# Optimization experiments

Measured on AMD Instinct MI355X. Metric: run time of the kernel, lower is better.

Reference implementation:

```python
import jax, jax.numpy as jnp
import numpy as np

FISTA_ITER = 50
LAMBDA = 0.1
POWER_ITER = 100


def power_method(W):
    # Estimates c = largest eigenvalue of W^T W (squared spectral norm).
    # Torch code uses a random init vector; we use a fixed key for determinism.
    X0 = jax.random.normal(jax.random.key(1), (1, W.shape[1]), dtype=W.dtype)

    def body(i, carry):
        X, _ = carry
        X = (X @ W.T) @ W            # [1, m]
        nm = jnp.linalg.norm(X)
        return (X / nm, nm)

    _, nm = jax.lax.fori_loop(0, POWER_ITER, body, (X0, jnp.asarray(1.0, W.dtype)))
    return nm


def soft_threshold(X, lam):
    return jnp.sign(X) * jax.nn.relu(jnp.abs(X) - lam)


def fista(Y, W, lam, iters):
    c = power_method(W)
    eta = 1.0 / c
    Gamma0 = soft_threshold(Y @ (eta * W), lam)   # [B, m]
    Y_norm = jnp.linalg.norm(Y)
    t0 = jnp.asarray(1.0, Y.dtype)

    def step(carry, _):
        Gamma, Z, t = carry
        residual = Z @ W.T - Y                                   # [B, n]
        Gamma_new = soft_threshold(Z - eta * (residual @ W), lam / c)
        t_new = (1.0 + jnp.sqrt(1.0 + 4.0 * t ** 2)) / 2.0
        Z_new = Gamma_new + (t - 1.0) / t_new * (Gamma_new - Gamma)
        nrm = jnp.linalg.norm(residual) / Y_norm
        return (Gamma_new, Z_new, t_new), nrm

    (Gamma, _, _), norms = jax.lax.scan(step, (Gamma0, Gamma0, t0), None, length=iters)
    return Gamma, norms


def setup_inputs() -> dict:
    key = jax.random.key(0)
    k1, k2 = jax.random.split(key)
    Y = jax.random.normal(k1, (8192, 784), dtype=jnp.float32)
    W = jax.random.normal(k2, (784, 2048), dtype=jnp.float32)
    W = W / jnp.linalg.norm(W, axis=0, keepdims=True)  # NormDict
    return {"Y": Y, "W": W}


def reference(Y, W):
    Gamma, norms = fista(Y, W, LAMBDA, FISTA_ITER)
    X = Gamma @ W.T                  # reconstruction [B, 784]
    return (X, Gamma, norms)
```

## Files before the change

kernel.cpp:

```cpp
#include <hip/hip_runtime.h>
#include <math.h>

#define B_DIM   8192
#define N_DIM   784
#define NPAD    800
#define NROWS_W 1024
#define M_DIM   2048
#define XSZ     (B_DIM*N_DIM)
#define GSZ     (B_DIM*M_DIM)
#define NITER   50
#define PITER   100

typedef __attribute__((ext_vector_type(8))) short short8;
typedef __attribute__((ext_vector_type(4))) float floatx4;

__device__ __forceinline__ void async_ld16(const unsigned short* g, unsigned short* l){
  __builtin_amdgcn_global_load_lds(
      (const __attribute__((address_space(1))) unsigned int*)g,
      (__attribute__((address_space(3))) unsigned int*)l,
      16, 0, 0);
}

__device__ __forceinline__ unsigned rotl32(unsigned x, int d){ return (x<<d)|(x>>(32-d)); }

__device__ void threefry2x32(unsigned& v0, unsigned& v1){
  const unsigned ks0=0u, ks1=1u, ks2=0x1BD11BDBu;
  unsigned x0=v0+ks0, x1=v1+ks1;
#define RND(R) { x0+=x1; x1=rotl32(x1,R); x1^=x0; }
  RND(13) RND(15) RND(26) RND(6)
  x0+=ks1; x1+=ks2+1u;
  RND(17) RND(29) RND(16) RND(24)
  x0+=ks2; x1+=ks0+2u;
  RND(13) RND(15) RND(26) RND(6)
  x0+=ks0; x1+=ks1+3u;
  RND(17) RND(29) RND(16) RND(24)
  x0+=ks1; x1+=ks2+4u;
  RND(13) RND(15) RND(26) RND(6)
  x0+=ks2; x1+=ks0+5u;
#undef RND
  v0=x0; v1=x1;
}

__device__ float erfinv_f(float x){
  float w = -logf((1.0f-x)*(1.0f+x));
  float p;
  if (w < 5.0f){
    w -= 2.5f;
    p = 2.81022636e-08f;
    p = fmaf(p,w, 3.43273939e-07f);
    p = fmaf(p,w,-3.5233877e-06f);
    p = fmaf(p,w,-4.39150654e-06f);
    p = fmaf(p,w, 0.00021858087f);
    p = fmaf(p,w,-0.00125372503f);
    p = fmaf(p,w,-0.00417768164f);
    p = fmaf(p,w, 0.246640727f);
    p = fmaf(p,w, 1.50140941f);
  } else {
    w = sqrtf(w) - 3.0f;
    p = -0.000200214257f;
    p = fmaf(p,w, 0.000100950558f);
    p = fmaf(p,w, 0.00134934322f);
    p = fmaf(p,w,-0.00367342844f);
    p = fmaf(p,w, 0.00573950773f);
    p = fmaf(p,w,-0.0076224613f);
    p = fmaf(p,w, 0.00943887047f);
    p = fmaf(p,w, 1.00167406f);
    p = fmaf(p,w, 2.83297682f);
  }
  return p*x;
}

__device__ float bits_to_normal(unsigned b){
  unsigned fb = (b>>9) | 0x3f800000u;
  float u01 = __uint_as_float(fb) - 1.0f;
  const float lo = -0.99999994f;
  float u = u01*(1.0f - lo) + lo;
  u = fmaxf(lo, u);
  return 1.41421356237f * erfinv_f(u);
}

__global__ void setup_kernel(float* __restrict__ xbuf0, float* __restrict__ accs){
  int i = threadIdx.x;
  if (i < 64) accs[i] = 0.0f;
  unsigned v0 = (unsigned)i, v1 = (unsigned)(1024+i);
  threefry2x32(v0, v1);
  xbuf0[i]        = bits_to_normal(v0);
  xbuf0[1024 + i] = bits_to_normal(v1);
}

__device__ __forceinline__ unsigned short f2bf(float f){
  unsigned u = __float_as_uint(f);
  unsigned r = (u + 0x7fffu + ((u>>16)&1u)) >> 16;
  return (unsigned short)r;
}
__device__ __forceinline__ unsigned pack2(float a, float b){
  return (unsigned)f2bf(a) | ((unsigned)f2bf(b) << 16);
}
__device__ __forceinline__ float bf2f(unsigned short s){
  return __uint_as_float(((unsigned)s) << 16);
}

__global__ void conv_w(const float* __restrict__ W, unsigned short* __restrict__ Wbf){
  int i4 = (blockIdx.x*256 + threadIdx.x)*4;
  int row = i4 >> 11;
  uint2 p = make_uint2(0,0);
  if (row < N_DIM){
    float4 v = *(const float4*)(W + (size_t)row*M_DIM + (i4 & 2047));
    p.x = pack2(v.x, v.y); p.y = pack2(v.z, v.w);
  }
  *(uint2*)(Wbf + i4) = p;
}

__global__ void conv_y(const float* __restrict__ Y, unsigned short* __restrict__ Ybf){
  int row = blockIdx.x;
  int c4 = threadIdx.x*4;
  if (c4 >= NPAD) return;
  uint2 p = make_uint2(0,0);
  if (c4 < N_DIM){
    float4 v = *(const float4*)(Y + (size_t)row*N_DIM + c4);
    p.x = pack2(v.x, v.y); p.y = pack2(v.z, v.w);
  }
  *(uint2*)(Ybf + (size_t)row*NPAD + c4) = p;
}

__global__ void transpose_w(const float* __restrict__ W, unsigned short* __restrict__ WTbf){
  __shared__ float tile[32][33];
  int k0 = blockIdx.x*32;
  int j0 = blockIdx.y*32;
  int tx = threadIdx.x & 31, ty = threadIdx.x >> 5;
#pragma unroll
  for (int i=0;i<4;i++){
    int j = j0 + ty + 8*i;
    float v = (j < N_DIM) ? W[(size_t)j*M_DIM + k0 + tx] : 0.0f;
    tile[tx][ty+8*i] = v;
  }
  __syncthreads();
#pragma unroll
  for (int i=0;i<4;i++){
    int k = k0 + ty + 8*i;
    WTbf[(size_t)k*NPAD + j0 + tx] = f2bf(tile[ty+8*i][tx]);
  }
}

__global__ __launch_bounds__(256)
void compute_q(const float* __restrict__ W, float* __restrict__ Q){
  __shared__ float As2[16][132];
  __shared__ float Bs2[16][132];
  const int t = threadIdx.x;
  const int a0 = blockIdx.x*128, b0 = blockIdx.y*128;
  const int ty = t>>4, tx = t&15;
  float acc[8][8];
#pragma unroll
  for (int i=0;i<8;i++)
#pragma unroll
    for (int j=0;j<8;j++) acc[i][j]=0.0f;

  for (int j0=0; j0<N_DIM; j0+=16){
#pragma unroll
    for (int h=0; h<8; ++h){
      int idx = h*256 + t;
      int r = idx>>7, c = idx&127;
      As2[r][c] = W[(size_t)(j0+r)*M_DIM + a0 + c];
      Bs2[r][c] = W[(size_t)(j0+r)*M_DIM + b0 + c];
    }
    __syncthreads();
#pragma unroll
    for (int kk=0; kk<16; ++kk){
      float a[8], b[8];
#pragma unroll
      for (int i=0;i<8;i++) a[i] = As2[kk][ty*8+i];
#pragma unroll
      for (int j=0;j<8;j++) b[j] = Bs2[kk][tx*8+j];
#pragma unroll
      for (int i=0;i<8;i++)
#pragma unroll
        for (int j=0;j<8;j++) acc[i][j] = fmaf(a[i], b[j], acc[i][j]);
    }
    __syncthreads();
  }
#pragma unroll
  for (int i=0;i<8;i++){
    int a = a0 + ty*8 + i;
#pragma unroll
    for (int j=0;j<8;j++) Q[(size_t)a*M_DIM + b0 + tx*8 + j] = acc[i][j];
  }
}

__global__ void sumsq_kernel(const float* __restrict__ v, int n, float* __restrict__ acc){
  __shared__ float red[256];
  int t = threadIdx.x;
  float s = 0.0f;
  for (int i = blockIdx.x*256 + t; i < n; i += gridDim.x*256){ float x = v[i]; s = fmaf(x,x,s); }
  red[t] = s; __syncthreads();
  for (int off=128; off>0; off>>=1){ if (t<off) red[t]+=red[t+off]; __syncthreads(); }
  if (t==0) atomicAdd(acc, red[0]);
}

__global__ void pm_q(const float* __restrict__ x, const float* __restrict__ Q,
                     float* __restrict__ xout){
  __shared__ float red[256];
  int t = threadIdx.x;
  float s = 0.0f;
  for (int k=t; k<M_DIM; k+=256){ float v = x[k]; s = fmaf(v,v,s); }
  red[t]=s; __syncthreads();
  for (int off=128; off>0; off>>=1){ if (t<off) red[t]+=red[t+off]; __syncthreads(); }
  float inv = 1.0f/sqrtf(red[0]);
  int wave = t>>6, lane = t&63;
  int j = blockIdx.x*4 + wave;
  const float* Qr = Q + (size_t)j*M_DIM;
  float acc = 0.0f;
  for (int k=lane; k<M_DIM; k+=64) acc = fmaf(x[k], Qr[k], acc);
  for (int off=32; off>0; off>>=1) acc += __shfl_down(acc, off);
  if (lane==0) xout[j] = acc * inv;
}

__global__ void finish_power(const float* __restrict__ xfin, const float* __restrict__ accs,
                             float* __restrict__ params){
  __shared__ float red[256];
  int t = threadIdx.x;
  float s = 0.0f;
  for (int k=t; k<M_DIM; k+=256){ float v = xfin[k]; s = fmaf(v,v,s); }
  red[t]=s; __syncthreads();
  for (int off=128; off>0; off>>=1){ if (t<off) red[t]+=red[t+off]; __syncthreads(); }
  if (t==0){
    float c = sqrtf(red[0]);
    params[0] = c;
    params[1] = 1.0f/c;
    params[2] = 0.1f/c;
    params[3] = sqrtf(accs[0]);
  }
}

__device__ __forceinline__ float softthr(float v, float th){
  float a = fmaxf(fabsf(v) - th, 0.0f);
  return copysignf(a, v);
}

template<int MODE>
__global__ __launch_bounds__(256)
void mfma_nt(const unsigned short* __restrict__ Abf,
             const unsigned short* __restrict__ Bbf,
             const float* __restrict__ Y,
             unsigned short* __restrict__ Rbf,
             float* __restrict__ X,
             float* __restrict__ nacc){
  __shared__ float4 smem4[2560];
  unsigned short* As0 = (unsigned short*)smem4;
  unsigned short* Bs0 = As0 + 64*32;
  unsigned short* As1 = Bs0 + 256*32;
  unsigned short* Bs1 = As1 + 64*32;
  float* fbuf = (float*)smem4;

  const int bid = blockIdx.x;
  const int g8  = bid & 7, w = bid >> 3;
  const int m0  = (g8*16 + (w>>2))*64;
  const int n0  = (w & 3)*256;

  const int t    = threadIdx.x;
  const int wave = t>>6, lane = t&63;
  const int wm2  = wave>>1, wn2 = wave&1;
  const int quad = lane>>4, l15 = lane&15;
  const int lrow = lane>>2;
  const int lk   = (lane&3)*8;

  floatx4 acc[2][8];
#pragma unroll
  for (int i=0;i<2;i++)
#pragma unroll
    for (int j=0;j<8;j++) acc[i][j] = (floatx4)(0.0f);

  auto stage = [&](unsigned short* As, unsigned short* Bs, int k0){
    async_ld16(Abf + (size_t)(m0 + wave*16 + lrow)*M_DIM + k0 + lk, &As[wave*512]);
#pragma unroll
    for (int c=0; c<4; ++c){
      int chunk = wave*4 + c;
      async_ld16(Bbf + (size_t)(n0 + chunk*16 + lrow)*M_DIM + k0 + lk, &Bs[chunk*512]);
    }
  };

  stage(As0, Bs0, 0);
  __syncthreads();
  int cur = 0;
  for (int k0=0; k0<M_DIM; k0+=32, cur^=1){
    unsigned short* As = cur ? As1 : As0;
    unsigned short* Bs = cur ? Bs1 : Bs0;
    if (k0+32 < M_DIM) stage(cur ? As0 : As1, cur ? Bs0 : Bs1, k0+32);
    short8 af[2], bfr[8];
#pragma unroll
    for (int ti=0; ti<2; ++ti)
      af[ti] = *(const short8*)&As[(wm2*32 + ti*16 + l15)*32 + quad*8];
#pragma unroll
    for (int tj=0; tj<8; ++tj)
      bfr[tj] = *(const short8*)&Bs[(wn2*128 + tj*16 + l15)*32 + quad*8];
#pragma unroll
    for (int ti=0; ti<2; ++ti)
#pragma unroll
      for (int tj=0; tj<8; ++tj)
        acc[ti][tj] = __builtin_amdgcn_mfma_f32_16x16x32_bf16(af[ti], bfr[tj], acc[ti][tj], 0, 0, 0);
    __syncthreads();
  }

  float ss = 0.0f;
#pragma unroll
  for (int c=0; c<4; ++c){
    if (wn2 == (c>>1)){
      int tb = (c&1)*4;
#pragma unroll
      for (int ti=0; ti<2; ++ti)
#pragma unroll
        for (int u=0; u<4; ++u)
#pragma unroll
          for (int r=0; r<4; ++r)
            fbuf[(wm2*32 + ti*16 + quad*4 + r)*68 + u*16 + l15] = acc[ti][tb+u][r];
    }
    __syncthreads();
#pragma unroll
    for (int k=0; k<4; ++k){
      int row = k*16 + (t>>4);
      int col = (t&15)*4;
      int m = m0 + row;
      int n = n0 + c*64 + col;
      float4 v = *(const float4*)&fbuf[row*68 + col];
      if (MODE==0){
        if (n < N_DIM){
          float4 yv = *(const float4*)(Y + (size_t)m*N_DIM + n);
          float r0 = v.x - yv.x, r1 = v.y - yv.y, r2 = v.z - yv.z, r3 = v.w - yv.w;
          uint2 p; p.x = pack2(r0, r1); p.y = pack2(r2, r3);
          *(uint2*)(Rbf + (size_t)m*NPAD + n) = p;
          ss = fmaf(r0,r0, fmaf(r1,r1, fmaf(r2,r2, fmaf(r3,r3, ss))));
        } else if (n < NPAD){
          *(uint2*)(Rbf + (size_t)m*NPAD + n) = make_uint2(0,0);
        }
      } else {
        if (n < N_DIM) *(float4*)(X + (size_t)m*N_DIM + n) = v;
      }
    }
    __syncthreads();
  }

  if (MODE==0){
    for (int off=32; off>0; off>>=1) ss += __shfl_down(ss, off);
    if (lane==0) atomicAdd(nacc, ss);
  }
}

template<int MODE>
__global__ __launch_bounds__(256,3)
void mfma_nn(const unsigned short* __restrict__ Abf,
             const unsigned short* __restrict__ WTbf,
             float* __restrict__ Gamma,
             unsigned short* __restrict__ Zhi,
             unsigned short* __restrict__ Zlo,
             const float* __restrict__ params,
             float mu){
  __shared__ float4 smem4[2048];
  unsigned short* As0 = (unsigned short*)smem4;
  unsigned short* Bs0 = As0 + 128*32;
  unsigned short* As1 = Bs0 + 128*32;
  unsigned short* Bs1 = As1 + 128*32;
  float* fbuf = (float*)smem4;

  const int bid = blockIdx.x;
  const int g8  = bid & 7, w = bid >> 3;
  const int m0  = (g8*8 + (w>>4))*128;
  const int n0  = (w & 15)*128;

  const int t    = threadIdx.x;
  const int wave = t>>6, lane = t&63;
  const int wm   = wave>>1, wn = wave&1;
  const int quad = lane>>4, l15 = lane&15;
  const int lrow = lane>>2;
  const int lk   = (lane&3)*8;

  floatx4 acc[4][4];
#pragma unroll
  for (int i=0;i<4;i++)
#pragma unroll
    for (int j=0;j<4;j++) acc[i][j] = (floatx4)(0.0f);

  auto stage = [&](unsigned short* As, unsigned short* Bs, int k0){
#pragma unroll
    for (int c=0; c<2; ++c){
      int chunk = wave*2 + c;
      async_ld16(Abf  + (size_t)(m0 + chunk*16 + lrow)*NPAD + k0 + lk, &As[chunk*512]);
      async_ld16(WTbf + (size_t)(n0 + chunk*16 + lrow)*NPAD + k0 + lk, &Bs[chunk*512]);
    }
  };

  stage(As0, Bs0, 0);
  __syncthreads();
  int cur = 0;
  for (int k0=0; k0<NPAD; k0+=32, cur^=1){
    unsigned short* As = cur ? As1 : As0;
    unsigned short* Bs = cur ? Bs1 : Bs0;
    if (k0+32 < NPAD) stage(cur ? As0 : As1, cur ? Bs0 : Bs1, k0+32);
    short8 af[4], bfr[4];
#pragma unroll
    for (int ti=0; ti<4; ++ti)
      af[ti] = *(const short8*)&As[(wm*64 + ti*16 + l15)*32 + quad*8];
#pragma unroll
    for (int tj=0; tj<4; ++tj)
      bfr[tj] = *(const short8*)&Bs[(wn*64 + tj*16 + l15)*32 + quad*8];
#pragma unroll
    for (int ti=0; ti<4; ++ti)
#pragma unroll
      for (int tj=0; tj<4; ++tj)
        acc[ti][tj] = __builtin_amdgcn_mfma_f32_16x16x32_bf16(af[ti], bfr[tj], acc[ti][tj], 0, 0, 0);
    __syncthreads();
  }

  const float eta  = params[1];
  const float lamc = params[2];

#pragma unroll
  for (int c=0; c<4; ++c){
    if (wn == (c>>1)){
      int tb = (c&1)*2;
#pragma unroll
      for (int ti=0; ti<4; ++ti)
#pragma unroll
        for (int u=0; u<2; ++u)
#pragma unroll
          for (int r=0; r<4; ++r)
            fbuf[(wm*64 + ti*16 + quad*4 + r)*36 + u*16 + l15] = acc[ti][tb+u][r];
    }
    __syncthreads();
    const int rbase = t>>3;
    const int col   = (t&7)*4;
    const int n     = n0 + c*32 + col;
    size_t idx[4];
    uint2 ph[4], pl[4];
    float4 gov[4];
#pragma unroll
    for (int k=0; k<4; ++k){
      int m = m0 + k*32 + rbase;
      idx[k] = (size_t)m*M_DIM + n;
      if (MODE!=0){
        ph[k] = *(const uint2*)(Zhi + idx[k]);
        pl[k] = *(const uint2*)(Zlo + idx[k]);
      }
      if (MODE==1) gov[k] = *(const float4*)(Gamma + idx[k]);
    }
#pragma unroll
    for (int k=0; k<4; ++k){
      int row = k*32 + rbase;
      float4 g4 = *(const float4*)&fbuf[row*36 + col];
      float gr[4] = {g4.x, g4.y, g4.z, g4.w};
      if (MODE!=0){
        unsigned short h[4] = {(unsigned short)(ph[k].x&0xffff),(unsigned short)(ph[k].x>>16),
                               (unsigned short)(ph[k].y&0xffff),(unsigned short)(ph[k].y>>16)};
        unsigned short l[4] = {(unsigned short)(pl[k].x&0xffff),(unsigned short)(pl[k].x>>16),
                               (unsigned short)(pl[k].y&0xffff),(unsigned short)(pl[k].y>>16)};
#pragma unroll
        for (int e=0;e<4;e++){
          float zv = bf2f(h[e]) + bf2f(l[e]);
          gr[e] = softthr(zv - eta*gr[e], lamc);
        }
      } else {
#pragma unroll
        for (int e=0;e<4;e++) gr[e] = softthr(eta*gr[e], 0.1f);
      }
      *(float4*)(Gamma + idx[k]) = make_float4(gr[0],gr[1],gr[2],gr[3]);
      if (MODE==1){
        float go0 = gov[k].x, go1 = gov[k].y, go2 = gov[k].z, go3 = gov[k].w;
        float zn[4];
        zn[0] = gr[0] + mu*(gr[0] - go0);
        zn[1] = gr[1] + mu*(gr[1] - go1);
        zn[2] = gr[2] + mu*(gr[2] - go2);
        zn[3] = gr[3] + mu*(gr[3] - go3);
        unsigned short h0=f2bf(zn[0]), h1=f2bf(zn[1]), h2=f2bf(zn[2]), h3=f2bf(zn[3]);
        uint2 phx; phx.x = (unsigned)h0 | ((unsigned)h1<<16); phx.y = (unsigned)h2 | ((unsigned)h3<<16);
        uint2 plx; plx.x = pack2(zn[0]-bf2f(h0), zn[1]-bf2f(h1));
                   plx.y = pack2(zn[2]-bf2f(h2), zn[3]-bf2f(h3));
        *(uint2*)(Zhi + idx[k]) = phx;
        *(uint2*)(Zlo + idx[k]) = plx;
      } else if (MODE==0){
        unsigned short h0=f2bf(gr[0]), h1=f2bf(gr[1]), h2=f2bf(gr[2]), h3=f2bf(gr[3]);
        uint2 phx; phx.x = (unsigned)h0 | ((unsigned)h1<<16); phx.y = (unsigned)h2 | ((unsigned)h3<<16);
        uint2 plx; plx.x = pack2(gr[0]-bf2f(h0), gr[1]-bf2f(h1));
                   plx.y = pack2(gr[2]-bf2f(h2), gr[3]-bf2f(h3));
        *(uint2*)(Zhi + idx[k]) = phx;
        *(uint2*)(Zlo + idx[k]) = plx;
      } else {
        uint2 phx; phx.x = pack2(gr[0], gr[1]); phx.y = pack2(gr[2], gr[3]);
        *(uint2*)(Zhi + idx[k]) = phx;
      }
    }
    __syncthreads();
  }
}

__global__ void norms_finalize(const float* __restrict__ nacc, const float* __restrict__ params,
                               float* __restrict__ out){
  int i = threadIdx.x;
  if (i < NITER) out[i] = sqrtf(nacc[i]) / params[3];
}

extern "C" void kernel_launch(void* const* d_in, const int* in_sizes, int n_in,
                              void* d_out, int out_size, void* d_ws, size_t ws_size,
                              hipStream_t stream){
  const float* Y  = (const float*)d_in[0];
  const float* W  = (const float*)d_in[1];
  float* out      = (float*)d_out;
  float* X        = out;
  float* Gamma    = out + XSZ;
  float* norms    = out + XSZ + GSZ;

  unsigned short* Zhi  = (unsigned short*)d_ws;
  unsigned short* Zlo  = Zhi  + (size_t)GSZ;
  unsigned short* Rbf  = Zlo  + (size_t)GSZ;
  unsigned short* Wbf  = Rbf  + (size_t)B_DIM*NPAD;
  unsigned short* WTbf = Wbf  + (size_t)NROWS_W*M_DIM;
  float* Q      = (float*)(WTbf + (size_t)M_DIM*NPAD);
  float* xb0    = Q + (size_t)M_DIM*M_DIM;
  float* xb1    = xb0 + M_DIM;
  float* params = xb1 + M_DIM;
  float* accs   = params + 8;

  setup_kernel<<<dim3(1), dim3(1024), 0, stream>>>(xb0, accs);
  sumsq_kernel<<<dim3(512), dim3(256), 0, stream>>>(Y, XSZ, accs);
  conv_w      <<<dim3(2048), dim3(256), 0, stream>>>(W, Wbf);
  transpose_w <<<dim3(64,25), dim3(256), 0, stream>>>(W, WTbf);
  conv_y      <<<dim3(B_DIM), dim3(256), 0, stream>>>(Y, Rbf);

  compute_q<<<dim3(16,16), dim3(256), 0, stream>>>(W, Q);
  float* xa = xb0; float* xc = xb1;
  for (int it=0; it<PITER; ++it){
    pm_q<<<dim3(512), dim3(256), 0, stream>>>(xa, Q, xc);
    float* tmp = xa; xa = xc; xc = tmp;
  }
  finish_power<<<dim3(1), dim3(256), 0, stream>>>(xa, accs, params);

  mfma_nn<0><<<dim3(1024), dim3(256), 0, stream>>>(Rbf, WTbf, Gamma, Zhi, Zlo, params, 0.0f);

  float tcur = 1.0f;
  for (int it=0; it<NITER; ++it){
    mfma_nt<0><<<dim3(512), dim3(256), 0, stream>>>(Zhi, Wbf, Y, Rbf, nullptr, accs + 1 + it);
    float tsq = tcur*tcur;
    float tn  = (1.0f + sqrtf(1.0f + 4.0f*tsq)) / 2.0f;
    float mu  = (tcur - 1.0f) / tn;
    tcur = tn;
    if (it < NITER-1)
      mfma_nn<1><<<dim3(1024), dim3(256), 0, stream>>>(Rbf, WTbf, Gamma, Zhi, Zlo, params, mu);
    else
      mfma_nn<2><<<dim3(1024), dim3(256), 0, stream>>>(Rbf, WTbf, Gamma, Zhi, Zlo, params, mu);
  }

  norms_finalize<<<dim3(1), dim3(64), 0, stream>>>(accs + 1, params, norms);

  mfma_nt<1><<<dim3(512), dim3(256), 0, stream>>>(Zhi, Wbf, nullptr, nullptr, X, nullptr);
}
```

Baseline: 8.316 ms.

## Shrink power-method Gram matrix, swizzle LDS tiles, keep fp32 Z/Gamma in fragment layout

The power method now iterates on the 784x784 matrix W W^T instead of the 2048x2048 W^T W. It tracks the Rayleigh quotient through atomics, so each iteration no longer needs its own norm reduction. Both MFMA GEMMs use an XOR swizzle on the LDS k-offset to cut bank conflicts. The FISTA epilogue keeps fp32 Z and Gamma in a per-thread fragment layout (Gamma scratch lives in the output buffer), which removes the LDS transpose and the hi/lo bf16 split except in the final iteration. The costs are scattered 2-byte Zhi stores and a different eigenvalue estimator whose numerics may differ slightly.

```diff
diff --git a/kernel.cpp b/kernel.cpp
--- a/kernel.cpp
+++ b/kernel.cpp
@@ -79,9 +79,11 @@
   return 1.41421356237f * erfinv_f(u);
 }
 
-__global__ void setup_kernel(float* __restrict__ xbuf0, float* __restrict__ accs){
+__global__ void setup_kernel(float* __restrict__ xbuf0, float* __restrict__ accs,
+                             float* __restrict__ dbuf){
   int i = threadIdx.x;
   if (i < 64) accs[i] = 0.0f;
+  if (i < 128) dbuf[i] = (i==0) ? 1.0f : 0.0f;
   unsigned v0 = (unsigned)i, v1 = (unsigned)(1024+i);
   threefry2x32(v0, v1);
   xbuf0[i]        = bits_to_normal(v0);
@@ -143,47 +145,91 @@
 }
 
 __global__ __launch_bounds__(256)
-void compute_q(const float* __restrict__ W, float* __restrict__ Q){
-  __shared__ float As2[16][132];
-  __shared__ float Bs2[16][132];
+void compute_qp(const float* __restrict__ W, float* __restrict__ Qp){
+  __shared__ float As2[64][33];
+  __shared__ float Bs2[64][33];
   const int t = threadIdx.x;
-  const int a0 = blockIdx.x*128, b0 = blockIdx.y*128;
+  const int a0 = blockIdx.x*64, b0 = blockIdx.y*64;
   const int ty = t>>4, tx = t&15;
-  float acc[8][8];
-#pragma unroll
-  for (int i=0;i<8;i++)
-#pragma unroll
-    for (int j=0;j<8;j++) acc[i][j]=0.0f;
-
-  for (int j0=0; j0<N_DIM; j0+=16){
-#pragma unroll
-    for (int h=0; h<8; ++h){
-      int idx = h*256 + t;
-      int r = idx>>7, c = idx&127;
-      As2[r][c] = W[(size_t)(j0+r)*M_DIM + a0 + c];
-      Bs2[r][c] = W[(size_t)(j0+r)*M_DIM + b0 + c];
-    }
-    __syncthreads();
-#pragma unroll
-    for (int kk=0; kk<16; ++kk){
-      float a[8], b[8];
-#pragma unroll
-      for (int i=0;i<8;i++) a[i] = As2[kk][ty*8+i];
-#pragma unroll
-      for (int j=0;j<8;j++) b[j] = Bs2[kk][tx*8+j];
-#pragma unroll
-      for (int i=0;i<8;i++)
-#pragma unroll
-        for (int j=0;j<8;j++) acc[i][j] = fmaf(a[i], b[j], acc[i][j]);
-    }
-    __syncthreads();
-  }
-#pragma unroll
-  for (int i=0;i<8;i++){
-    int a = a0 + ty*8 + i;
-#pragma unroll
-    for (int j=0;j<8;j++) Q[(size_t)a*M_DIM + b0 + tx*8 + j] = acc[i][j];
-  }
+  float acc[4][4];
+#pragma unroll
+  for (int i=0;i<4;i++)
+#pragma unroll
+    for (int j=0;j<4;j++) acc[i][j]=0.0f;
+
+  for (int k0=0; k0<M_DIM; k0+=32){
+#pragma unroll
+    for (int h=0; h<2; ++h){
+      int row = h*32 + (t>>3);
+      int kq  = (t&7)*4;
+      float4 av = make_float4(0,0,0,0), bv = make_float4(0,0,0,0);
+      if (a0+row < N_DIM) av = *(const float4*)(W + (size_t)(a0+row)*M_DIM + k0 + kq);
+      if (b0+row < N_DIM) bv = *(const float4*)(W + (size_t)(b0+row)*M_DIM + k0 + kq);
+      As2[row][kq]=av.x; As2[row][kq+1]=av.y; As2[row][kq+2]=av.z; As2[row][kq+3]=av.w;
+      Bs2[row][kq]=bv.x; Bs2[row][kq+1]=bv.y; Bs2[row][kq+2]=bv.z; Bs2[row][kq+3]=bv.w;
+    }
+    __syncthreads();
+#pragma unroll
+    for (int kk=0; kk<32; ++kk){
+      float a[4], b[4];
+#pragma unroll
+      for (int i=0;i<4;i++) a[i] = As2[ty*4+i][kk];
+#pragma unroll
+      for (int j=0;j<4;j++) b[j] = Bs2[tx*4+j][kk];
+#pragma unroll
+      for (int i=0;i<4;i++)
+#pragma unroll
+        for (int j=0;j<4;j++) acc[i][j] = fmaf(a[i], b[j], acc[i][j]);
+    }
+    __syncthreads();
+  }
+#pragma unroll
+  for (int i=0;i<4;i++){
+    int a = a0 + ty*4 + i;
+    if (a >= N_DIM) continue;
+#pragma unroll
+    for (int j=0;j<4;j++){
+      int b = b0 + tx*4 + j;
+      if (b < N_DIM) Qp[(size_t)a*N_DIM + b] = acc[i][j];
+    }
+  }
+}
+
+__global__ void u0_kernel(const float* __restrict__ x0, const float* __restrict__ W,
+                          float* __restrict__ u0){
+  int wave = threadIdx.x>>6, lane = threadIdx.x&63;
+  int j = blockIdx.x*4 + wave;
+  const float* Wr = W + (size_t)j*M_DIM;
+  float s = 0.0f;
+  for (int k=lane; k<M_DIM; k+=64) s = fmaf(x0[k], Wr[k], s);
+  for (int off=32; off>0; off>>=1) s += __shfl_down(s, off);
+  if (lane==0) u0[j] = s;
+}
+
+__global__ void pm_qp(const float* __restrict__ vin, const float* __restrict__ din,
+                      const float* __restrict__ Qp,
+                      float* __restrict__ vout, float* __restrict__ dout){
+  int wave = threadIdx.x>>6, lane = threadIdx.x&63;
+  int j = blockIdx.x*4 + wave;
+  float inv = 1.0f/sqrtf(*din);
+  const float* Qr = Qp + (size_t)j*N_DIM;
+  float s = 0.0f;
+  for (int k=lane; k<N_DIM; k+=64) s = fmaf(vin[k], Qr[k], s);
+  for (int off=32; off>0; off>>=1) s += __shfl_down(s, off);
+  if (lane==0){
+    float w = s * inv;
+    vout[j] = w;
+    atomicAdd(dout, w * vin[j] * inv);
+  }
+}
+
+__global__ void finish_power2(const float* __restrict__ d100, const float* __restrict__ accs,
+                              float* __restrict__ params){
+  float c = sqrtf(*d100);
+  params[0] = c;
+  params[1] = 1.0f/c;
+  params[2] = 0.1f/c;
+  params[3] = sqrtf(accs[0]);
 }
 
 __global__ void sumsq_kernel(const float* __restrict__ v, int n, float* __restrict__ acc){
@@ -194,41 +240,6 @@
   red[t] = s; __syncthreads();
   for (int off=128; off>0; off>>=1){ if (t<off) red[t]+=red[t+off]; __syncthreads(); }
   if (t==0) atomicAdd(acc, red[0]);
-}
-
-__global__ void pm_q(const float* __restrict__ x, const float* __restrict__ Q,
-                     float* __restrict__ xout){
-  __shared__ float red[256];
-  int t = threadIdx.x;
-  float s = 0.0f;
-  for (int k=t; k<M_DIM; k+=256){ float v = x[k]; s = fmaf(v,v,s); }
-  red[t]=s; __syncthreads();
-  for (int off=128; off>0; off>>=1){ if (t<off) red[t]+=red[t+off]; __syncthreads(); }
-  float inv = 1.0f/sqrtf(red[0]);
-  int wave = t>>6, lane = t&63;
-  int j = blockIdx.x*4 + wave;
-  const float* Qr = Q + (size_t)j*M_DIM;
-  float acc = 0.0f;
-  for (int k=lane; k<M_DIM; k+=64) acc = fmaf(x[k], Qr[k], acc);
-  for (int off=32; off>0; off>>=1) acc += __shfl_down(acc, off);
-  if (lane==0) xout[j] = acc * inv;
-}
-
-__global__ void finish_power(const float* __restrict__ xfin, const float* __restrict__ accs,
-                             float* __restrict__ params){
-  __shared__ float red[256];
-  int t = threadIdx.x;
-  float s = 0.0f;
-  for (int k=t; k<M_DIM; k+=256){ float v = xfin[k]; s = fmaf(v,v,s); }
-  red[t]=s; __syncthreads();
-  for (int off=128; off>0; off>>=1){ if (t<off) red[t]+=red[t+off]; __syncthreads(); }
-  if (t==0){
-    float c = sqrtf(red[0]);
-    params[0] = c;
-    params[1] = 1.0f/c;
-    params[2] = 0.1f/c;
-    params[3] = sqrtf(accs[0]);
-  }
 }
 
 __device__ __forceinline__ float softthr(float v, float th){
@@ -261,7 +272,8 @@
   const int wm2  = wave>>1, wn2 = wave&1;
   const int quad = lane>>4, l15 = lane&15;
   const int lrow = lane>>2;
-  const int lk   = (lane&3)*8;
+  const int lks  = ((lane&3) ^ ((lrow>>1)&3))*8;
+  const int ksw  = (quad ^ ((l15>>1)&3))*8;
 
   floatx4 acc[2][8];
 #pragma unroll
@@ -270,11 +282,11 @@
     for (int j=0;j<8;j++) acc[i][j] = (floatx4)(0.0f);
 
   auto stage = [&](unsigned short* As, unsigned short* Bs, int k0){
-    async_ld16(Abf + (size_t)(m0 + wave*16 + lrow)*M_DIM + k0 + lk, &As[wave*512]);
+    async_ld16(Abf + (size_t)(m0 + wave*16 + lrow)*M_DIM + k0 + lks, &As[wave*512]);
 #pragma unroll
     for (int c=0; c<4; ++c){
       int chunk = wave*4 + c;
-      async_ld16(Bbf + (size_t)(n0 + chunk*16 + lrow)*M_DIM + k0 + lk, &Bs[chunk*512]);
+      async_ld16(Bbf + (size_t)(n0 + chunk*16 + lrow)*M_DIM + k0 + lks, &Bs[chunk*512]);
     }
   };
 
@@ -288,10 +300,10 @@
     short8 af[2], bfr[8];
 #pragma unroll
     for (int ti=0; ti<2; ++ti)
-      af[ti] = *(const short8*)&As[(wm2*32 + ti*16 + l15)*32 + quad*8];
+      af[ti] = *(const short8*)&As[(wm2*32 + ti*16 + l15)*32 + ksw];
 #pragma unroll
     for (int tj=0; tj<8; ++tj)
-      bfr[tj] = *(const short8*)&Bs[(wn2*128 + tj*16 + l15)*32 + quad*8];
+      bfr[tj] = *(const short8*)&Bs[(wn2*128 + tj*16 + l15)*32 + ksw];
 #pragma unroll
     for (int ti=0; ti<2; ++ti)
 #pragma unroll
@@ -350,7 +362,8 @@
              const unsigned short* __restrict__ WTbf,
              float* __restrict__ Gamma,
              unsigned short* __restrict__ Zhi,
-             unsigned short* __restrict__ Zlo,
+             float* __restrict__ Zf,
+             float* __restrict__ Gf,
              const float* __restrict__ params,
              float mu){
   __shared__ float4 smem4[2048];
@@ -370,7 +383,8 @@
   const int wm   = wave>>1, wn = wave&1;
   const int quad = lane>>4, l15 = lane&15;
   const int lrow = lane>>2;
-  const int lk   = (lane&3)*8;
+  const int lks  = ((lane&3) ^ ((lrow>>1)&3))*8;
+  const int ksw  = (quad ^ ((l15>>1)&3))*8;
 
   floatx4 acc[4][4];
 #pragma unroll
@@ -382,8 +396,8 @@
 #pragma unroll
     for (int c=0; c<2; ++c){
       int chunk = wave*2 + c;
-      async_ld16(Abf  + (size_t)(m0 + chunk*16 + lrow)*NPAD + k0 + lk, &As[chunk*512]);
-      async_ld16(WTbf + (size_t)(n0 + chunk*16 + lrow)*NPAD + k0 + lk, &Bs[chunk*512]);
+      async_ld16(Abf  + (size_t)(m0 + chunk*16 + lrow)*NPAD + k0 + lks, &As[chunk*512]);
+      async_ld16(WTbf + (size_t)(n0 + chunk*16 + lrow)*NPAD + k0 + lks, &Bs[chunk*512]);
     }
   };
 
@@ -397,10 +411,10 @@
     short8 af[4], bfr[4];
 #pragma unroll
     for (int ti=0; ti<4; ++ti)
-      af[ti] = *(const short8*)&As[(wm*64 + ti*16 + l15)*32 + quad*8];
+      af[ti] = *(const short8*)&As[(wm*64 + ti*16 + l15)*32 + ksw];
 #pragma unroll
     for (int tj=0; tj<4; ++tj)
-      bfr[tj] = *(const short8*)&Bs[(wn*64 + tj*16 + l15)*32 + quad*8];
+      bfr[tj] = *(const short8*)&Bs[(wn*64 + tj*16 + l15)*32 + ksw];
 #pragma unroll
     for (int ti=0; ti<4; ++ti)
 #pragma unroll
@@ -411,82 +425,85 @@
 
   const float eta  = params[1];
   const float lamc = params[2];
-
-#pragma unroll
-  for (int c=0; c<4; ++c){
-    if (wn == (c>>1)){
-      int tb = (c&1)*2;
-#pragma unroll
-      for (int ti=0; ti<4; ++ti)
-#pragma unroll
-        for (int u=0; u<2; ++u)
-#pragma unroll
-          for (int r=0; r<4; ++r)
-            fbuf[(wm*64 + ti*16 + quad*4 + r)*36 + u*16 + l15] = acc[ti][tb+u][r];
-    }
-    __syncthreads();
-    const int rbase = t>>3;
-    const int col   = (t&7)*4;
-    const int n     = n0 + c*32 + col;
-    size_t idx[4];
-    uint2 ph[4], pl[4];
-    float4 gov[4];
-#pragma unroll
-    for (int k=0; k<4; ++k){
-      int m = m0 + k*32 + rbase;
-      idx[k] = (size_t)m*M_DIM + n;
-      if (MODE!=0){
-        ph[k] = *(const uint2*)(Zhi + idx[k]);
-        pl[k] = *(const uint2*)(Zlo + idx[k]);
+  const size_t blockL = (size_t)((m0>>7)*16 + (n0>>7));
+  float* GfB = Gf + blockL*16384 + (size_t)t*4;
+  float* ZfB = Zf + blockL*16384 + (size_t)t*4;
+  const int mrow0 = m0 + wm*64 + quad*4;
+  const int ncol  = n0 + wn*64 + l15;
+
+  if (MODE==2){
+#pragma unroll
+    for (int ti=0; ti<4; ++ti)
+#pragma unroll
+      for (int tj=0; tj<4; ++tj){
+        float4 zf4 = *(const float4*)(ZfB + (ti*4+tj)*1024);
+        acc[ti][tj][0] = softthr(zf4.x - eta*acc[ti][tj][0], lamc);
+        acc[ti][tj][1] = softthr(zf4.y - eta*acc[ti][tj][1], lamc);
+        acc[ti][tj][2] = softthr(zf4.z - eta*acc[ti][tj][2], lamc);
+        acc[ti][tj][3] = softthr(zf4.w - eta*acc[ti][tj][3], lamc);
       }
-      if (MODE==1) gov[k] = *(const float4*)(Gamma + idx[k]);
-    }
-#pragma unroll
-    for (int k=0; k<4; ++k){
-      int row = k*32 + rbase;
-      float4 g4 = *(const float4*)&fbuf[row*36 + col];
-      float gr[4] = {g4.x, g4.y, g4.z, g4.w};
-      if (MODE!=0){
-        unsigned short h[4] = {(unsigned short)(ph[k].x&0xffff),(unsigned short)(ph[k].x>>16),
-                               (unsigned short)(ph[k].y&0xffff),(unsigned short)(ph[k].y>>16)};
-        unsigned short l[4] = {(unsigned short)(pl[k].x&0xffff),(unsigned short)(pl[k].x>>16),
-                               (unsigned short)(pl[k].y&0xffff),(unsigned short)(pl[k].y>>16)};
-#pragma unroll
-        for (int e=0;e<4;e++){
-          float zv = bf2f(h[e]) + bf2f(l[e]);
-          gr[e] = softthr(zv - eta*gr[e], lamc);
+    __syncthreads();
+#pragma unroll
+    for (int c=0; c<4; ++c){
+      if (wn == (c>>1)){
+        int tb = (c&1)*2;
+#pragma unroll
+        for (int ti=0; ti<4; ++ti)
+#pragma unroll
+          for (int u=0; u<2; ++u)
+#pragma unroll
+            for (int r=0; r<4; ++r)
+              fbuf[(wm*64 + ti*16 + quad*4 + r)*36 + u*16 + l15] = acc[ti][tb+u][r];
+      }
+      __syncthreads();
+#pragma unroll
+      for (int k=0; k<4; ++k){
+        int row = k*32 + (t>>3);
+        int col = (t&7)*4;
+        int m = m0 + row;
+        int n = n0 + c*32 + col;
+        size_t idx = (size_t)m*M_DIM + n;
+        float4 g4 = *(const float4*)&fbuf[row*36 + col];
+        *(float4*)(Gamma + idx) = g4;
+        uint2 phx; phx.x = pack2(g4.x, g4.y); phx.y = pack2(g4.z, g4.w);
+        *(uint2*)(Zhi + idx) = phx;
+      }
+      __syncthreads();
+    }
+  } else {
+#pragma unroll
+    for (int ti=0; ti<4; ++ti){
+      float4 go4[4], zf4[4];
+      if (MODE==1){
+#pragma unroll
+        for (int tj=0; tj<4; ++tj) go4[tj] = *(const float4*)(GfB + (ti*4+tj)*1024);
+#pragma unroll
+        for (int tj=0; tj<4; ++tj) zf4[tj] = *(const float4*)(ZfB + (ti*4+tj)*1024);
+      }
+#pragma unroll
+      for (int tj=0; tj<4; ++tj){
+        float gr[4], zn[4];
+        if (MODE==1){
+          float z[4]  = {zf4[tj].x, zf4[tj].y, zf4[tj].z, zf4[tj].w};
+          float go[4] = {go4[tj].x, go4[tj].y, go4[tj].z, go4[tj].w};
+#pragma unroll
+          for (int r=0;r<4;r++){
+            gr[r] = softthr(z[r] - eta*acc[ti][tj][r], lamc);
+            zn[r] = gr[r] + mu*(gr[r] - go[r]);
+          }
+        } else {
+#pragma unroll
+          for (int r=0;r<4;r++){ gr[r] = softthr(eta*acc[ti][tj][r], 0.1f); zn[r] = gr[r]; }
         }
-      } else {
-#pragma unroll
-        for (int e=0;e<4;e++) gr[e] = softthr(eta*gr[e], 0.1f);
+        *(float4*)(GfB + (ti*4+tj)*1024) = make_float4(gr[0],gr[1],gr[2],gr[3]);
+        *(float4*)(ZfB + (ti*4+tj)*1024) = make_float4(zn[0],zn[1],zn[2],zn[3]);
+        size_t zb = (size_t)(mrow0 + ti*16)*M_DIM + ncol + tj*16;
+        Zhi[zb]            = f2bf(zn[0]);
+        Zhi[zb + M_DIM]    = f2bf(zn[1]);
+        Zhi[zb + 2*M_DIM]  = f2bf(zn[2]);
+        Zhi[zb + 3*M_DIM]  = f2bf(zn[3]);
       }
-      *(float4*)(Gamma + idx[k]) = make_float4(gr[0],gr[1],gr[2],gr[3]);
-      if (MODE==1){
-        float go0 = gov[k].x, go1 = gov[k].y, go2 = gov[k].z, go3 = gov[k].w;
-        float zn[4];
-        zn[0] = gr[0] + mu*(gr[0] - go0);
-        zn[1] = gr[1] + mu*(gr[1] - go1);
-        zn[2] = gr[2] + mu*(gr[2] - go2);
-        zn[3] = gr[3] + mu*(gr[3] - go3);
-        unsigned short h0=f2bf(zn[0]), h1=f2bf(zn[1]), h2=f2bf(zn[2]), h3=f2bf(zn[3]);
-        uint2 phx; phx.x = (unsigned)h0 | ((unsigned)h1<<16); phx.y = (unsigned)h2 | ((unsigned)h3<<16);
-        uint2 plx; plx.x = pack2(zn[0]-bf2f(h0), zn[1]-bf2f(h1));
-                   plx.y = pack2(zn[2]-bf2f(h2), zn[3]-bf2f(h3));
-        *(uint2*)(Zhi + idx[k]) = phx;
-        *(uint2*)(Zlo + idx[k]) = plx;
-      } else if (MODE==0){
-        unsigned short h0=f2bf(gr[0]), h1=f2bf(gr[1]), h2=f2bf(gr[2]), h3=f2bf(gr[3]);
-        uint2 phx; phx.x = (unsigned)h0 | ((unsigned)h1<<16); phx.y = (unsigned)h2 | ((unsigned)h3<<16);
-        uint2 plx; plx.x = pack2(gr[0]-bf2f(h0), gr[1]-bf2f(h1));
-                   plx.y = pack2(gr[2]-bf2f(h2), gr[3]-bf2f(h3));
-        *(uint2*)(Zhi + idx[k]) = phx;
-        *(uint2*)(Zlo + idx[k]) = plx;
-      } else {
-        uint2 phx; phx.x = pack2(gr[0], gr[1]); phx.y = pack2(gr[2], gr[3]);
-        *(uint2*)(Zhi + idx[k]) = phx;
-      }
-    }
-    __syncthreads();
+    }
   }
 }
 
@@ -507,31 +524,36 @@
   float* norms    = out + XSZ + GSZ;
 
   unsigned short* Zhi  = (unsigned short*)d_ws;
-  unsigned short* Zlo  = Zhi  + (size_t)GSZ;
-  unsigned short* Rbf  = Zlo  + (size_t)GSZ;
+  float* Zf            = (float*)(Zhi + (size_t)GSZ);
+  unsigned short* Rbf  = (unsigned short*)(Zf + (size_t)GSZ);
   unsigned short* Wbf  = Rbf  + (size_t)B_DIM*NPAD;
   unsigned short* WTbf = Wbf  + (size_t)NROWS_W*M_DIM;
-  float* Q      = (float*)(WTbf + (size_t)M_DIM*NPAD);
-  float* xb0    = Q + (size_t)M_DIM*M_DIM;
-  float* xb1    = xb0 + M_DIM;
-  float* params = xb1 + M_DIM;
+  float* Qp     = (float*)(WTbf + (size_t)M_DIM*NPAD);
+  float* w0     = Qp + (size_t)N_DIM*N_DIM;
+  float* w1     = w0 + 1024;
+  float* dbuf   = w1 + 1024;
+  float* params = dbuf + 128;
   float* accs   = params + 8;
-
-  setup_kernel<<<dim3(1), dim3(1024), 0, stream>>>(xb0, accs);
+  float* xb0    = accs + 64;
+
+  float* Gf = Gamma;
+
+  setup_kernel<<<dim3(1), dim3(1024), 0, stream>>>(xb0, accs, dbuf);
   sumsq_kernel<<<dim3(512), dim3(256), 0, stream>>>(Y, XSZ, accs);
   conv_w      <<<dim3(2048), dim3(256), 0, stream>>>(W, Wbf);
   transpose_w <<<dim3(64,25), dim3(256), 0, stream>>>(W, WTbf);
   conv_y      <<<dim3(B_DIM), dim3(256), 0, stream>>>(Y, Rbf);
 
-  compute_q<<<dim3(16,16), dim3(256), 0, stream>>>(W, Q);
-  float* xa = xb0; float* xc = xb1;
-  for (int it=0; it<PITER; ++it){
-    pm_q<<<dim3(512), dim3(256), 0, stream>>>(xa, Q, xc);
-    float* tmp = xa; xa = xc; xc = tmp;
-  }
-  finish_power<<<dim3(1), dim3(256), 0, stream>>>(xa, accs, params);
-
-  mfma_nn<0><<<dim3(1024), dim3(256), 0, stream>>>(Rbf, WTbf, Gamma, Zhi, Zlo, params, 0.0f);
+  compute_qp<<<dim3(13,13), dim3(256), 0, stream>>>(W, Qp);
+  u0_kernel <<<dim3(196), dim3(256), 0, stream>>>(xb0, W, w0);
+  float* va = w0; float* vb = w1;
+  for (int it=1; it<=PITER; ++it){
+    pm_qp<<<dim3(196), dim3(256), 0, stream>>>(va, dbuf + it - 1, Qp, vb, dbuf + it);
+    float* tmp = va; va = vb; vb = tmp;
+  }
+  finish_power2<<<dim3(1), dim3(1), 0, stream>>>(dbuf + PITER, accs, params);
+
+  mfma_nn<0><<<dim3(1024), dim3(256), 0, stream>>>(Rbf, WTbf, Gamma, Zhi, Zf, Gf, params, 0.0f);
 
   float tcur = 1.0f;
   for (int it=0; it<NITER; ++it){
@@ -541,9 +563,9 @@
     float mu  = (tcur - 1.0f) / tn;
     tcur = tn;
     if (it < NITER-1)
-      mfma_nn<1><<<dim3(1024), dim3(256), 0, stream>>>(Rbf, WTbf, Gamma, Zhi, Zlo, params, mu);
+      mfma_nn<1><<<dim3(1024), dim3(256), 0, stream>>>(Rbf, WTbf, Gamma, Zhi, Zf, Gf, params, mu);
     else
-      mfma_nn<2><<<dim3(1024), dim3(256), 0, stream>>>(Rbf, WTbf, Gamma, Zhi, Zlo, params, mu);
+      mfma_nn<2><<<dim3(1024), dim3(256), 0, stream>>>(Rbf, WTbf, Gamma, Zhi, Zf, Gf, params, mu);
   }
 
   norms_finalize<<<dim3(1), dim3(64), 0, stream>>>(accs + 1, params, norms);
```

Result: slower. 8.931 ms (+7.4%).
